# Performance work log

Measured on AMD Instinct MI355X. Metric: run time of the kernel, lower is better.

## Reference

```python
import jax, jax.numpy as jnp
import numpy as np

B, S, D, O, C = 4, 2048, 1024, 1024, 8


def setup_inputs() -> dict:
    key = jax.random.key(0)
    k1, k2, k3, k4 = jax.random.split(key, 4)
    x = jax.random.normal(k1, (B, S, D), dtype=jnp.float32)
    category_id = jax.random.randint(k2, (B, S), 0, C, dtype=jnp.int64)
    weight = jax.random.normal(k3, (C, D, O), dtype=jnp.float32)
    bias = jax.random.normal(k4, (C, O), dtype=jnp.float32)
    return {"x": x, "category_id": category_id, "weight": weight, "bias": bias}


def reference(x, category_id, weight, bias):
    # Faithful to: out[t] = x[t] @ weight[cid[t]] + bias[cid[t]]
    # Instead of gathering a full [T, D, O] weight tensor per token (32GB),
    # compute every category's projection once and select per token.
    orig_shape = x.shape
    x_flat = x.reshape(-1, orig_shape[-1])          # [T, D]
    cid = category_id.reshape(-1)                    # [T]
    out_all = jnp.einsum('td,cdo->tco', x_flat, weight)  # [T, C, O]
    out = jnp.take_along_axis(out_all, cid[:, None, None], axis=1)[:, 0, :]  # [T, O]
    out = out + bias[cid]
    return out.reshape(orig_shape[:-1] + (weight.shape[-1],))
```

## Files before the change

kernel.cpp:

```cpp
#include <hip/hip_runtime.h>

#define TOK   8192
#define DIM   1024
#define OUTD  1024
#define NCAT  8
#define BM    128
#define BN    128
#define BK    32
#define NKT   (DIM / BK)
#define MAX_MT 71
#define MPMAX (MAX_MT * BM)

typedef __attribute__((ext_vector_type(8))) __bf16 bf16x8;
typedef __attribute__((ext_vector_type(4))) float  f32x4;

#define GLP(p)  (const __attribute__((address_space(1))) unsigned int*)(p)
#define LDSP(p) (__attribute__((address_space(3))) unsigned int*)(p)

__device__ __forceinline__ unsigned short f2bf(float f) {
  unsigned u = __float_as_uint(f);
  u += 0x7fffu + ((u >> 16) & 1u);
  return (unsigned short)(u >> 16);
}

__global__ __launch_bounds__(256) void k_prep(const float* __restrict__ w,
    const int* __restrict__ cid, unsigned short* __restrict__ wt,
    int* __restrict__ row_token, int* __restrict__ tile_c, int* __restrict__ tile_m) {
  int tid = threadIdx.x;
  if (blockIdx.x < 2048) {
    int b = blockIdx.x;
    int ot = b & 15, dt = (b >> 4) & 15, c = b >> 8;
    __shared__ unsigned short t[64][72];
    int i  = tid >> 2;
    int jg = tid & 3;
    const float* src = w + ((size_t)c << 20) + (size_t)(dt * 64 + i) * 1024 + ot * 64 + jg * 16;
    #pragma unroll
    for (int q = 0; q < 4; ++q) {
      float4 v = *(const float4*)(src + q * 4);
      t[jg * 16 + q * 4 + 0][i] = f2bf(v.x);
      t[jg * 16 + q * 4 + 1][i] = f2bf(v.y);
      t[jg * 16 + q * 4 + 2][i] = f2bf(v.z);
      t[jg * 16 + q * 4 + 3][i] = f2bf(v.w);
    }
    __syncthreads();
    unsigned short* dst = wt + ((size_t)c << 20) + (size_t)(ot * 64 + i) * 1024 + dt * 64 + jg * 16;
    uint4 a = *(const uint4*)&t[i][jg * 16];
    uint4 bq = *(const uint4*)&t[i][jg * 16 + 8];
    *(uint4*)dst = a;
    *(uint4*)(dst + 8) = bq;
    return;
  }

  __shared__ int wcnt[4][NCAT];
  __shared__ int wbase[4][NCAT];
  __shared__ int gbase[NCAT];
  int lane = tid & 63, wave = tid >> 6;
  int base = wave * 2048;

  int cs[32];
  #pragma unroll
  for (int it = 0; it < 32; ++it) cs[it] = cid[base + it * 64 + lane];
  int cnt_loc[NCAT];
  #pragma unroll
  for (int c = 0; c < NCAT; ++c) cnt_loc[c] = 0;
  #pragma unroll
  for (int it = 0; it < 32; ++it)
    #pragma unroll
    for (int c = 0; c < NCAT; ++c)
      cnt_loc[c] += __popcll(__ballot(cs[it] == c));
  if (lane == 0) {
    #pragma unroll
    for (int c = 0; c < NCAT; ++c) wcnt[wave][c] = cnt_loc[c];
  }
  __syncthreads();

  if (tid == 0) {
    int pr = 0, mt = 0;
    for (int c = 0; c < NCAT; ++c) {
      int tot = 0;
      for (int wv = 0; wv < 4; ++wv) { wbase[wv][c] = tot; tot += wcnt[wv][c]; }
      gbase[c] = pr;
      int nt = (tot + BM - 1) / BM;
      for (int i = 0; i < nt; ++i) { tile_c[mt] = c; tile_m[mt] = pr + i * BM; ++mt; }
      pr += nt * BM;
    }
    for (; mt < MAX_MT; ++mt) { tile_c[mt] = -1; tile_m[mt] = 0; }
  }
  __syncthreads();
  for (int r = tid; r < MPMAX; r += 256) row_token[r] = -1;
  __syncthreads();

  int run[NCAT];
  #pragma unroll
  for (int c = 0; c < NCAT; ++c) run[c] = gbase[c] + wbase[wave][c];
  unsigned long long lt = (lane == 63) ? ~0ull >> 1 : ((1ull << lane) - 1);
  #pragma unroll
  for (int it = 0; it < 32; ++it) {
    int c = cs[it];
    int pos = 0;
    #pragma unroll
    for (int cat = 0; cat < NCAT; ++cat) {
      unsigned long long m = __ballot(cs[it] == cat);
      if (cat == c) pos = run[cat] + __popcll(m & lt);
      run[cat] += __popcll(m);
    }
    row_token[pos] = base + it * 64 + lane;
  }
}

__global__ __launch_bounds__(256) void k_gemm(const float* __restrict__ x,
    const unsigned short* __restrict__ wt, const float* __restrict__ bias,
    const int* __restrict__ row_token, const int* __restrict__ tile_c,
    const int* __restrict__ tile_m, float* __restrict__ out) {
  int wg  = blockIdx.x;
  int lin = (wg & 7) * MAX_MT + (wg >> 3);
  int mt  = lin >> 3;
  int nt  = lin & 7;
  int c = tile_c[mt];
  if (c < 0) return;
  int m0 = tile_m[mt];
  int n0 = nt * BN;

  __shared__ unsigned short As[3][BM][BK];
  __shared__ unsigned short Bs[3][BM][BK];

  int tid  = threadIdx.x;
  int lane = tid & 63;
  int wr = (tid >> 6) >> 1, wc = (tid >> 6) & 1;

  f32x4 acc[4][4];
  #pragma unroll
  for (int m = 0; m < 4; ++m)
    #pragma unroll
    for (int n = 0; n < 4; ++n) acc[m][n] = (f32x4){0.f, 0.f, 0.f, 0.f};

  int ra = tid >> 1;
  int kh = (tid & 1) << 4;
  int tokA = row_token[m0 + ra];
  const float* xs = x + (size_t)(tokA < 0 ? 0 : tokA) * DIM + kh;
  int aw = (ra >> 1) & 3;
  int g0 = (tid & 1) << 1;
  int a0 = ((g0 ^ aw) << 3);
  int a1 = (((g0 + 1) ^ aw) << 3);

  int srow = tid >> 2;
  int sdst = (tid & 3) << 3;
  int gsrc = (((tid & 3) ^ ((tid >> 3) & 3)) << 3);
  const unsigned short* Bg = wt + ((size_t)c << 20) + (size_t)n0 * DIM;

  auto STAGE_B = [&](int b, int kt) {
    __builtin_amdgcn_global_load_lds(GLP(Bg + (size_t)srow * DIM + kt + gsrc),
                                     LDSP(&Bs[b][srow][sdst]), 16, 0, 0);
    __builtin_amdgcn_global_load_lds(GLP(Bg + (size_t)(srow + 64) * DIM + kt + gsrc),
                                     LDSP(&Bs[b][srow + 64][sdst]), 16, 0, 0);
  };

  float4 sA0[4], sA1[4];
  auto AISSUE = [&](float4 (&s)[4], int t) {
    const float* p = xs + t * BK;
    #pragma unroll
    for (int q = 0; q < 4; ++q) s[q] = *(const float4*)(p + 4 * q);
  };
  auto AWRITE = [&](float4 (&s)[4], int b) {
    bf16x8 p0, p1;
    p0[0] = (__bf16)s[0].x; p0[1] = (__bf16)s[0].y; p0[2] = (__bf16)s[0].z; p0[3] = (__bf16)s[0].w;
    p0[4] = (__bf16)s[1].x; p0[5] = (__bf16)s[1].y; p0[6] = (__bf16)s[1].z; p0[7] = (__bf16)s[1].w;
    p1[0] = (__bf16)s[2].x; p1[1] = (__bf16)s[2].y; p1[2] = (__bf16)s[2].z; p1[3] = (__bf16)s[2].w;
    p1[4] = (__bf16)s[3].x; p1[5] = (__bf16)s[3].y; p1[6] = (__bf16)s[3].z; p1[7] = (__bf16)s[3].w;
    if (tokA < 0) { p0 = (bf16x8){}; p1 = (bf16x8){}; }
    *(bf16x8*)&As[b][ra][a0] = p0;
    *(bf16x8*)&As[b][ra][a1] = p1;
  };

  int rcol = (((lane >> 4) ^ (((lane & 15) >> 1) & 3)) << 3);
  int arow = wr * 64 + (lane & 15);
  int brow = wc * 64 + (lane & 15);

  STAGE_B(0, 0);      AISSUE(sA0, 0);
  STAGE_B(1, BK);     AISSUE(sA1, 1);
  asm volatile("s_waitcnt vmcnt(6)" ::: "memory");
  AWRITE(sA0, 0);
  asm volatile("s_waitcnt lgkmcnt(0)" ::: "memory");
  __builtin_amdgcn_s_barrier();

  auto BODY = [&](int t, float4 (&sI)[4], float4 (&sW)[4]) {
    bool pre2 = (t + 2 < NKT);
    bool pre1 = (t + 1 < NKT);
    if (pre2) { STAGE_B((t + 2) % 3, (t + 2) * BK); AISSUE(sI, t + 2); }

    int b = t % 3;
    bf16x8 af[4], bf[4];
    #pragma unroll
    for (int m = 0; m < 4; ++m)
      af[m] = *(const bf16x8*)&As[b][arow + m * 16][rcol];
    #pragma unroll
    for (int n = 0; n < 4; ++n)
      bf[n] = *(const bf16x8*)&Bs[b][brow + n * 16][rcol];
    #pragma unroll
    for (int m = 0; m < 4; ++m)
      #pragma unroll
      for (int n = 0; n < 4; ++n)
        acc[m][n] = __builtin_amdgcn_mfma_f32_16x16x32_bf16(af[m], bf[n], acc[m][n], 0, 0, 0);

    if (pre1) {
      if (pre2) asm volatile("s_waitcnt vmcnt(6)" ::: "memory");
      else      asm volatile("s_waitcnt vmcnt(0)" ::: "memory");
      AWRITE(sW, (t + 1) % 3);
      asm volatile("s_waitcnt lgkmcnt(0)" ::: "memory");
      __builtin_amdgcn_s_barrier();
    }
  };
  for (int t2 = 0; t2 < NKT; t2 += 2) {
    BODY(t2,     sA0, sA1);
    BODY(t2 + 1, sA1, sA0);
  }

  int col = lane & 15;
  int rq  = (lane >> 4) << 2;
  float bv[4];
  #pragma unroll
  for (int n = 0; n < 4; ++n) bv[n] = bias[c * OUTD + n0 + wc * 64 + n * 16 + col];
  #pragma unroll
  for (int m = 0; m < 4; ++m) {
    #pragma unroll
    for (int r = 0; r < 4; ++r) {
      int prow = m0 + wr * 64 + m * 16 + rq + r;
      int tok = row_token[prow];
      if (tok < 0) continue;
      float* orow = out + (size_t)tok * OUTD + n0 + wc * 64 + col;
      #pragma unroll
      for (int n = 0; n < 4; ++n) orow[n * 16] = acc[m][n][r] + bv[n];
    }
  }
}

extern "C" void kernel_launch(void* const* d_in, const int* in_sizes, int n_in,
                              void* d_out, int out_size, void* d_ws, size_t ws_size,
                              hipStream_t stream) {
  const float* x    = (const float*)d_in[0];
  const int*   cid  = (const int*)d_in[1];
  const float* w    = (const float*)d_in[2];
  const float* bias = (const float*)d_in[3];
  float* out = (float*)d_out;

  char* ws = (char*)d_ws;
  constexpr size_t WT_BYTES = (size_t)NCAT * DIM * OUTD * 2;
  constexpr size_t RT_BYTES = (size_t)MPMAX * 4;
  unsigned short* wtb = (unsigned short*)ws;
  int* row_token = (int*)(ws + WT_BYTES);
  int* tile_c    = (int*)(ws + WT_BYTES + RT_BYTES);
  int* tile_m    = tile_c + MAX_MT;

  k_prep<<<2049, 256, 0, stream>>>(w, cid, wtb, row_token, tile_c, tile_m);
  k_gemm<<<8 * MAX_MT, 256, 0, stream>>>(x, wtb, bias, row_token, tile_c, tile_m, out);
}
```

Measured before the change: 180.5 us.

## Pre-convert activations to bf16 and stage A tiles via direct global-to-LDS loads

Adds a pass in the prep kernel that converts x to bf16 in a workspace buffer. The GEMM then loads gathered A rows with global_load_lds like the weight tiles, instead of loading fp32 into registers and converting each k-step. The pipeline becomes a single wait-and-barrier per iteration with a three-stage buffer. This removes per-tile conversion and register staging from the inner loop and halves the A traffic, at the cost of an extra bandwidth pass over x.

```diff
diff --git a/kernel.cpp b/kernel.cpp
--- a/kernel.cpp
+++ b/kernel.cpp
@@ -24,7 +24,8 @@
 }
 
 __global__ __launch_bounds__(256) void k_prep(const float* __restrict__ w,
-    const int* __restrict__ cid, unsigned short* __restrict__ wt,
+    const float* __restrict__ x, const int* __restrict__ cid,
+    unsigned short* __restrict__ wt, unsigned short* __restrict__ xb,
     int* __restrict__ row_token, int* __restrict__ tile_c, int* __restrict__ tile_m) {
   int tid = threadIdx.x;
   if (blockIdx.x < 2048) {
@@ -50,6 +51,16 @@
     *(uint4*)(dst + 8) = bq;
     return;
   }
+  if (blockIdx.x < 6144) {
+    size_t idx = ((size_t)(blockIdx.x - 2048) * 256 + tid) * 8;
+    const float4* s = (const float4*)(x + idx);
+    float4 a = s[0], b = s[1];
+    union { unsigned short u[8]; uint4 v; } o;
+    o.u[0] = f2bf(a.x); o.u[1] = f2bf(a.y); o.u[2] = f2bf(a.z); o.u[3] = f2bf(a.w);
+    o.u[4] = f2bf(b.x); o.u[5] = f2bf(b.y); o.u[6] = f2bf(b.z); o.u[7] = f2bf(b.w);
+    *(uint4*)(xb + idx) = o.v;
+    return;
+  }
 
   __shared__ int wcnt[4][NCAT];
   __shared__ int wbase[4][NCAT];
@@ -108,7 +119,7 @@
   }
 }
 
-__global__ __launch_bounds__(256) void k_gemm(const float* __restrict__ x,
+__global__ __launch_bounds__(256) void k_gemm(const unsigned short* __restrict__ xb,
     const unsigned short* __restrict__ wt, const float* __restrict__ bias,
     const int* __restrict__ row_token, const int* __restrict__ tile_c,
     const int* __restrict__ tile_m, float* __restrict__ out) {
@@ -134,59 +145,35 @@
     #pragma unroll
     for (int n = 0; n < 4; ++n) acc[m][n] = (f32x4){0.f, 0.f, 0.f, 0.f};
 
-  int ra = tid >> 1;
-  int kh = (tid & 1) << 4;
-  int tokA = row_token[m0 + ra];
-  const float* xs = x + (size_t)(tokA < 0 ? 0 : tokA) * DIM + kh;
-  int aw = (ra >> 1) & 3;
-  int g0 = (tid & 1) << 1;
-  int a0 = ((g0 ^ aw) << 3);
-  int a1 = (((g0 + 1) ^ aw) << 3);
-
   int srow = tid >> 2;
   int sdst = (tid & 3) << 3;
   int gsrc = (((tid & 3) ^ ((tid >> 3) & 3)) << 3);
-  const unsigned short* Bg = wt + ((size_t)c << 20) + (size_t)n0 * DIM;
-
-  auto STAGE_B = [&](int b, int kt) {
-    __builtin_amdgcn_global_load_lds(GLP(Bg + (size_t)srow * DIM + kt + gsrc),
-                                     LDSP(&Bs[b][srow][sdst]), 16, 0, 0);
-    __builtin_amdgcn_global_load_lds(GLP(Bg + (size_t)(srow + 64) * DIM + kt + gsrc),
-                                     LDSP(&Bs[b][srow + 64][sdst]), 16, 0, 0);
-  };
-
-  float4 sA0[4], sA1[4];
-  auto AISSUE = [&](float4 (&s)[4], int t) {
-    const float* p = xs + t * BK;
-    #pragma unroll
-    for (int q = 0; q < 4; ++q) s[q] = *(const float4*)(p + 4 * q);
-  };
-  auto AWRITE = [&](float4 (&s)[4], int b) {
-    bf16x8 p0, p1;
-    p0[0] = (__bf16)s[0].x; p0[1] = (__bf16)s[0].y; p0[2] = (__bf16)s[0].z; p0[3] = (__bf16)s[0].w;
-    p0[4] = (__bf16)s[1].x; p0[5] = (__bf16)s[1].y; p0[6] = (__bf16)s[1].z; p0[7] = (__bf16)s[1].w;
-    p1[0] = (__bf16)s[2].x; p1[1] = (__bf16)s[2].y; p1[2] = (__bf16)s[2].z; p1[3] = (__bf16)s[2].w;
-    p1[4] = (__bf16)s[3].x; p1[5] = (__bf16)s[3].y; p1[6] = (__bf16)s[3].z; p1[7] = (__bf16)s[3].w;
-    if (tokA < 0) { p0 = (bf16x8){}; p1 = (bf16x8){}; }
-    *(bf16x8*)&As[b][ra][a0] = p0;
-    *(bf16x8*)&As[b][ra][a1] = p1;
+
+  int tokA0 = row_token[m0 + srow];
+  int tokA1 = row_token[m0 + srow + 64];
+  const unsigned short* Ag0 = xb + (size_t)(tokA0 < 0 ? 0 : tokA0) * DIM + gsrc;
+  const unsigned short* Ag1 = xb + (size_t)(tokA1 < 0 ? 0 : tokA1) * DIM + gsrc;
+  const unsigned short* Bg  = wt + ((size_t)c << 20) + (size_t)n0 * DIM + gsrc;
+
+  auto STAGE = [&](int b, int kt) {
+    __builtin_amdgcn_global_load_lds(GLP(Ag0 + kt), LDSP(&As[b][srow][sdst]), 16, 0, 0);
+    __builtin_amdgcn_global_load_lds(GLP(Ag1 + kt), LDSP(&As[b][srow + 64][sdst]), 16, 0, 0);
+    __builtin_amdgcn_global_load_lds(GLP(Bg + (size_t)srow * DIM + kt), LDSP(&Bs[b][srow][sdst]), 16, 0, 0);
+    __builtin_amdgcn_global_load_lds(GLP(Bg + (size_t)(srow + 64) * DIM + kt), LDSP(&Bs[b][srow + 64][sdst]), 16, 0, 0);
   };
 
   int rcol = (((lane >> 4) ^ (((lane & 15) >> 1) & 3)) << 3);
   int arow = wr * 64 + (lane & 15);
   int brow = wc * 64 + (lane & 15);
 
-  STAGE_B(0, 0);      AISSUE(sA0, 0);
-  STAGE_B(1, BK);     AISSUE(sA1, 1);
-  asm volatile("s_waitcnt vmcnt(6)" ::: "memory");
-  AWRITE(sA0, 0);
-  asm volatile("s_waitcnt lgkmcnt(0)" ::: "memory");
-  __builtin_amdgcn_s_barrier();
-
-  auto BODY = [&](int t, float4 (&sI)[4], float4 (&sW)[4]) {
-    bool pre2 = (t + 2 < NKT);
-    bool pre1 = (t + 1 < NKT);
-    if (pre2) { STAGE_B((t + 2) % 3, (t + 2) * BK); AISSUE(sI, t + 2); }
+  STAGE(0, 0); STAGE(1, BK);
+
+  for (int t = 0; t < NKT; ++t) {
+    if (t < NKT - 1) asm volatile("s_waitcnt vmcnt(4) lgkmcnt(0)" ::: "memory");
+    else             asm volatile("s_waitcnt vmcnt(0) lgkmcnt(0)" ::: "memory");
+    __builtin_amdgcn_sched_barrier(0);
+    __builtin_amdgcn_s_barrier();
+    if (t + 2 < NKT) STAGE((t + 2) % 3, (t + 2) * BK);
 
     int b = t % 3;
     bf16x8 af[4], bf[4];
@@ -201,18 +188,6 @@
       #pragma unroll
       for (int n = 0; n < 4; ++n)
         acc[m][n] = __builtin_amdgcn_mfma_f32_16x16x32_bf16(af[m], bf[n], acc[m][n], 0, 0, 0);
-
-    if (pre1) {
-      if (pre2) asm volatile("s_waitcnt vmcnt(6)" ::: "memory");
-      else      asm volatile("s_waitcnt vmcnt(0)" ::: "memory");
-      AWRITE(sW, (t + 1) % 3);
-      asm volatile("s_waitcnt lgkmcnt(0)" ::: "memory");
-      __builtin_amdgcn_s_barrier();
-    }
-  };
-  for (int t2 = 0; t2 < NKT; t2 += 2) {
-    BODY(t2,     sA0, sA1);
-    BODY(t2 + 1, sA1, sA0);
   }
 
   int col = lane & 15;
@@ -244,13 +219,15 @@
   float* out = (float*)d_out;
 
   char* ws = (char*)d_ws;
+  constexpr size_t XB_BYTES = (size_t)TOK * DIM * 2;
   constexpr size_t WT_BYTES = (size_t)NCAT * DIM * OUTD * 2;
   constexpr size_t RT_BYTES = (size_t)MPMAX * 4;
-  unsigned short* wtb = (unsigned short*)ws;
-  int* row_token = (int*)(ws + WT_BYTES);
-  int* tile_c    = (int*)(ws + WT_BYTES + RT_BYTES);
+  unsigned short* xbb = (unsigned short*)ws;
+  unsigned short* wtb = (unsigned short*)(ws + XB_BYTES);
+  int* row_token = (int*)(ws + XB_BYTES + WT_BYTES);
+  int* tile_c    = (int*)(ws + XB_BYTES + WT_BYTES + RT_BYTES);
   int* tile_m    = tile_c + MAX_MT;
 
-  k_prep<<<2049, 256, 0, stream>>>(w, cid, wtb, row_token, tile_c, tile_m);
-  k_gemm<<<8 * MAX_MT, 256, 0, stream>>>(x, wtb, bias, row_token, tile_c, tile_m, out);
-}
+  k_prep<<<6145, 256, 0, stream>>>(w, x, cid, wtb, xbb, row_token, tile_c, tile_m);
+  k_gemm<<<8 * MAX_MT, 256, 0, stream>>>(xbb, wtb, bias, row_token, tile_c, tile_m, out);
+}
```

Result: faster. 156.9 us (-13.1%).
